# Kernel tuning notes

Hardware: AMD Instinct MI355X
Metric: run time of the kernel (lower is better)

Reference implementation:

```python
import jax, jax.numpy as jnp
import numpy as np

N = 100000   # nodes
E = 1600000  # edges
IN_DIM = 165
HID = 64
OUT = 2


def setup_inputs() -> dict:
    key = jax.random.key(0)
    ks = jax.random.split(key, 6)
    x = jax.random.normal(ks[0], (N, IN_DIM), dtype=jnp.float32)
    edge_index = jax.random.randint(ks[1], (2, E), 0, N, dtype=jnp.int32)
    # Glorot-ish init for the two GCNConv linear weights + post-agg biases
    W1 = jax.random.normal(ks[2], (IN_DIM, HID), dtype=jnp.float32) * (1.0 / np.sqrt(IN_DIM))
    b1 = jnp.zeros((HID,), dtype=jnp.float32)
    W2 = jax.random.normal(ks[3], (HID, OUT), dtype=jnp.float32) * (1.0 / np.sqrt(HID))
    b2 = jnp.zeros((OUT,), dtype=jnp.float32)
    return {"x": x, "edge_index": edge_index, "W1": W1, "b1": b1, "W2": W2, "b2": b2}


def _gcn_norm(src, dst, n):
    # PyG GCNConv default: add self-loops, symmetric normalization
    deg = jax.ops.segment_sum(jnp.ones_like(src, dtype=jnp.float32), dst, num_segments=n)
    deg = deg + 1.0  # self-loop
    dinv = jax.lax.rsqrt(deg)
    edge_norm = dinv[src] * dinv[dst]          # [E]
    self_norm = dinv * dinv                    # [N], norm for self-loop edges
    return edge_norm, self_norm


def _gcn_conv(h, W, b, src, dst, edge_norm, self_norm, n):
    hw = h @ W                                 # [N, F_out] transform first (PyG order)
    msgs = hw[src] * edge_norm[:, None]        # gather + scale  [E, F_out]
    agg = jax.ops.segment_sum(msgs, dst, num_segments=n)
    agg = agg + hw * self_norm[:, None]        # self-loop contribution
    return agg + b


def reference(x, edge_index, W1, b1, W2, b2):
    src, dst = edge_index[0], edge_index[1]
    edge_norm, self_norm = _gcn_norm(src, dst, N)
    h = _gcn_conv(x, W1, b1, src, dst, edge_norm, self_norm, N)
    h = jax.nn.relu(h)
    # F.dropout with training=False (eval) is identity
    out = _gcn_conv(h, W2, b2, src, dst, edge_norm, self_norm, N)
    return out
```

## Files before the change

### kernel.cpp

```cpp
#include <hip/hip_runtime.h>
#include <hip/hip_fp16.h>

#define N_NODES 100000
#define N_EDGES 1600000
#define IN_DIM 165
#define HID 64
#define OUT_DIM 2
#define NB ((N_NODES + 127) / 128)
#define CAP 3072
#define EPB 4096
#define BIN_BLOCKS ((N_EDGES + EPB - 1) / EPB)
#define KP 64
#define XST 72

typedef _Float16 f16x8 __attribute__((ext_vector_type(8)));
typedef float f32x4 __attribute__((ext_vector_type(4)));

__global__ __launch_bounds__(512) void k_bin(const int* __restrict__ src,
                                             const int* __restrict__ dst,
                                             int* __restrict__ bcnt,
                                             unsigned int* __restrict__ rec) {
    __shared__ int hist[NB];
    __shared__ int rstart[NB];
    __shared__ int gbase[NB];
    __shared__ int cur[NB];
    __shared__ int tsum[512];
    __shared__ unsigned int lrec[EPB];
    __shared__ unsigned short lbkt[EPB];
    const int tid = threadIdx.x;
    for (int b = tid; b < NB; b += 512) { hist[b] = 0; cur[b] = 0; }
    __syncthreads();
    const int e0 = blockIdx.x * EPB;
    const int total = min(EPB, N_EDGES - e0);
    for (int j = tid; j < total; j += 512)
        atomicAdd(&hist[dst[e0 + j] >> 7], 1);
    __syncthreads();
    int own[2];
    int s = 0;
    #pragma unroll
    for (int u = 0; u < 2; ++u) {
        int idx = tid * 2 + u;
        own[u] = s;
        s += (idx < NB) ? hist[idx] : 0;
    }
    tsum[tid] = s;
    __syncthreads();
    for (int off = 1; off < 512; off <<= 1) {
        int t = (tid >= off) ? tsum[tid - off] : 0;
        __syncthreads();
        tsum[tid] += t;
        __syncthreads();
    }
    int prev = (tid > 0) ? tsum[tid - 1] : 0;
    #pragma unroll
    for (int u = 0; u < 2; ++u) {
        int idx = tid * 2 + u;
        if (idx < NB) rstart[idx] = prev + own[u];
    }
    for (int b = tid; b < NB; b += 512)
        if (hist[b] > 0) gbase[b] = atomicAdd(&bcnt[b], hist[b]);
    __syncthreads();
    for (int j = tid; j < total; j += 512) {
        int d = dst[e0 + j], sv = src[e0 + j];
        int b = d >> 7;
        int off = atomicAdd(&cur[b], 1);
        int slot = rstart[b] + off;
        lrec[slot] = (unsigned int)sv | ((unsigned int)(d & 127) << 17);
        lbkt[slot] = (unsigned short)b;
    }
    __syncthreads();
    for (int slot = tid; slot < total; slot += 512) {
        int b = lbkt[slot];
        int pos = gbase[b] + (slot - rstart[b]);
        rec[(size_t)b * CAP + pos] = lrec[slot];
    }
}

__global__ void k_bscan(const int* __restrict__ bcnt, int* __restrict__ bbase,
                        int* __restrict__ row_ptr) {
    __shared__ int lds[1024];
    const int tid = threadIdx.x;
    int v = (tid < NB) ? bcnt[tid] : 0;
    lds[tid] = v;
    __syncthreads();
    for (int off = 1; off < 1024; off <<= 1) {
        int t = (tid >= off) ? lds[tid - off] : 0;
        __syncthreads();
        lds[tid] += t;
        __syncthreads();
    }
    if (tid < NB) bbase[tid] = lds[tid] - v;
    if (tid == 0) row_ptr[N_NODES] = N_EDGES;
}

__global__ __launch_bounds__(256) void k_sort2(const int* __restrict__ bcnt,
                                               const int* __restrict__ bbase,
                                               const unsigned int* __restrict__ rec,
                                               int* __restrict__ row_ptr,
                                               float* __restrict__ dinv,
                                               int* __restrict__ esrc) {
    __shared__ int hist[128];
    __shared__ int scn[128];
    __shared__ int cur[128];
    const int tid = threadIdx.x;
    const int b = blockIdx.x;
    const int n0 = b << 7;
    if (tid < 128) { hist[tid] = 0; cur[tid] = 0; }
    __syncthreads();
    const int cb = bcnt[b];
    const size_t s0 = (size_t)b * CAP;
    const int gb = bbase[b];
    unsigned int rv[12];
    #pragma unroll
    for (int u = 0; u < 12; ++u) {
        int i = tid + (u << 8);
        rv[u] = 0;
        if (i < cb) {
            rv[u] = rec[s0 + i];
            atomicAdd(&hist[rv[u] >> 17], 1);
        }
    }
    __syncthreads();
    int v = (tid < 128) ? hist[tid] : 0;
    if (tid < 128) scn[tid] = v;
    __syncthreads();
    for (int off = 1; off < 128; off <<= 1) {
        int t = (tid >= off && tid < 128) ? scn[tid - off] : 0;
        __syncthreads();
        if (tid < 128) scn[tid] += t;
        __syncthreads();
    }
    if (tid < 128) {
        int n = n0 + tid;
        if (n < N_NODES) {
            row_ptr[n] = gb + scn[tid] - v;
            dinv[n] = rsqrtf((float)v + 1.0f);
        }
    }
    __syncthreads();
    #pragma unroll
    for (int u = 0; u < 12; ++u) {
        int i = tid + (u << 8);
        if (i < cb) {
            int ld = (int)(rv[u] >> 17);
            int pos = gb + (scn[ld] - hist[ld]) + atomicAdd(&cur[ld], 1);
            esrc[pos] = (int)(rv[u] & 131071u);
        }
    }
}

__global__ __launch_bounds__(256) void k_gemm1(const float* __restrict__ x,
                                               const float* __restrict__ W1,
                                               const float* __restrict__ dinv,
                                               __half* __restrict__ hw1h) {
    __shared__ __align__(16) _Float16 xs[32 * XST];
    __shared__ __align__(16) _Float16 wsf[8 * 64 * 8];
    const int tid = threadIdx.x;
    const int lane = tid & 63;
    const int wave = tid >> 6;
    const int lg = lane >> 4;
    const int lm = lane & 15;
    const int mt = wave >> 1;
    const int nh = wave & 1;
    const int base = blockIdx.x * 32;
    const int nrows = min(32, N_NODES - base);

    const int srow = tid >> 3;
    const int sseg = (tid & 7) * 8;
    const int src_r = min(srow, nrows - 1);
    const float* xrow = x + (size_t)(base + src_r) * IN_DIM;
    const bool rvalid = (srow < nrows);

    f32x4 acc[2] = {};

    for (int p = 0; p < 3; ++p) {
        const int k0 = p * KP;
        #pragma unroll
        for (int u = 0; u < 8; ++u) {
            int kk = sseg + u;
            int k = k0 + kk;
            float v = xrow[min(k, IN_DIM - 1)];
            xs[srow * XST + kk] = (rvalid && k < IN_DIM) ? (_Float16)v : (_Float16)0.f;
        }
        #pragma unroll
        for (int it = 0; it < 2; ++it) {
            int idx = tid + 256 * it;
            int g = idx >> 6;
            int n = idx & 63;
            f16x8 frag;
            #pragma unroll
            for (int j = 0; j < 8; ++j) {
                int k = k0 + 8 * g + j;
                float v = W1[(size_t)min(k, IN_DIM - 1) * HID + n];
                frag[j] = (k < IN_DIM) ? (_Float16)v : (_Float16)0.f;
            }
            *(f16x8*)&wsf[((g << 6) + n) * 8] = frag;
        }
        __syncthreads();
        #pragma unroll
        for (int s = 0; s < 2; ++s) {
            f16x8 af = *(const f16x8*)&xs[(16 * mt + lm) * XST + 32 * s + 8 * lg];
            #pragma unroll
            for (int nb = 0; nb < 2; ++nb) {
                int nt = 2 * nh + nb;
                f16x8 bf = *(const f16x8*)&wsf[(((s << 2) + lg) * 64 + (nt << 4) + lm) * 8];
                acc[nb] = __builtin_amdgcn_mfma_f32_16x16x32_f16(af, bf, acc[nb], 0, 0, 0);
            }
        }
        __syncthreads();
    }

    #pragma unroll
    for (int r = 0; r < 4; ++r) {
        int grow = base + 16 * mt + 4 * lg + r;
        if (grow < N_NODES) {
            float dv = dinv[grow];
            #pragma unroll
            for (int nb = 0; nb < 2; ++nb) {
                int nt = 2 * nh + nb;
                hw1h[(size_t)grow * HID + (nt << 4) + lm] = __float2half(acc[nb][r] * dv);
            }
        }
    }
}

__global__ __launch_bounds__(256) void k_gather1(const int* __restrict__ row_ptr,
                                                 const int* __restrict__ esrc,
                                                 const __half* __restrict__ hw1h,
                                                 const float* __restrict__ dinv,
                                                 const float* __restrict__ b1,
                                                 const float* __restrict__ W2,
                                                 float* __restrict__ hw2s) {
    __shared__ float w2s[HID * OUT_DIM];
    __shared__ float b1s[HID];
    const int tid = threadIdx.x;
    if (tid < HID * OUT_DIM) w2s[tid] = W2[tid];
    if (tid < HID) b1s[tid] = b1[tid];
    __syncthreads();

    const int node = blockIdx.x * 16 + (tid >> 4);
    const int q = tid & 15;
    if (node >= N_NODES) return;
    const int beg = row_ptr[node], end = row_ptr[node + 1];
    float4 acc = {0.f, 0.f, 0.f, 0.f};
    int i = beg;
    for (; i + 7 < end; i += 8) {
        uint2 u[8];
        #pragma unroll
        for (int e = 0; e < 8; ++e) {
            int s = esrc[i + e];
            u[e] = *(const uint2*)&hw1h[(size_t)s * HID + 4 * q];
        }
        #pragma unroll
        for (int e = 0; e < 8; ++e) {
            float2 a0 = __half22float2(*(const __half2*)&u[e].x);
            float2 a1 = __half22float2(*(const __half2*)&u[e].y);
            acc.x += a0.x; acc.y += a0.y; acc.z += a1.x; acc.w += a1.y;
        }
    }
    for (; i + 3 < end; i += 4) {
        uint2 u[4];
        #pragma unroll
        for (int e = 0; e < 4; ++e) {
            int s = esrc[i + e];
            u[e] = *(const uint2*)&hw1h[(size_t)s * HID + 4 * q];
        }
        #pragma unroll
        for (int e = 0; e < 4; ++e) {
            float2 a0 = __half22float2(*(const __half2*)&u[e].x);
            float2 a1 = __half22float2(*(const __half2*)&u[e].y);
            acc.x += a0.x; acc.y += a0.y; acc.z += a1.x; acc.w += a1.y;
        }
    }
    for (; i < end; ++i) {
        int s = esrc[i];
        uint2 u = *(const uint2*)&hw1h[(size_t)s * HID + 4 * q];
        float2 a0 = __half22float2(*(const __half2*)&u.x);
        float2 a1 = __half22float2(*(const __half2*)&u.y);
        acc.x += a0.x; acc.y += a0.y; acc.z += a1.x; acc.w += a1.y;
    }
    const float dv = dinv[node];
    uint2 us = *(const uint2*)&hw1h[(size_t)node * HID + 4 * q];
    float2 h0 = __half22float2(*(const __half2*)&us.x);
    float2 h1 = __half22float2(*(const __half2*)&us.y);
    float h[4];
    h[0] = fmaxf(dv * (acc.x + h0.x) + b1s[4 * q + 0], 0.f);
    h[1] = fmaxf(dv * (acc.y + h0.y) + b1s[4 * q + 1], 0.f);
    h[2] = fmaxf(dv * (acc.z + h1.x) + b1s[4 * q + 2], 0.f);
    h[3] = fmaxf(dv * (acc.w + h1.y) + b1s[4 * q + 3], 0.f);
    float s0 = 0.f, s1 = 0.f;
    #pragma unroll
    for (int k = 0; k < 4; ++k) {
        int j = 4 * q + k;
        s0 += h[k] * w2s[2 * j + 0];
        s1 += h[k] * w2s[2 * j + 1];
    }
    #pragma unroll
    for (int off = 8; off >= 1; off >>= 1) {
        s0 += __shfl_down(s0, off, 16);
        s1 += __shfl_down(s1, off, 16);
    }
    if (q == 0) {
        hw2s[(size_t)node * 2 + 0] = s0 * dv;
        hw2s[(size_t)node * 2 + 1] = s1 * dv;
    }
}

__global__ __launch_bounds__(256) void k_gather2(const int* __restrict__ row_ptr,
                                                 const int* __restrict__ esrc,
                                                 const float* __restrict__ hw2s,
                                                 const float* __restrict__ dinv,
                                                 const float* __restrict__ b2,
                                                 float* __restrict__ out) {
    const int tid = threadIdx.x;
    const int node = blockIdx.x * 64 + (tid >> 2);
    const int e4 = tid & 3;
    if (node >= N_NODES) return;
    const int beg = row_ptr[node], end = row_ptr[node + 1];
    float a0 = 0.f, a1 = 0.f;
    for (int i = beg + e4; i < end; i += 4) {
        int s = esrc[i];
        float2 v = *(const float2*)&hw2s[(size_t)s * 2];
        a0 += v.x;
        a1 += v.y;
    }
    a0 += __shfl_xor(a0, 1, 4); a0 += __shfl_xor(a0, 2, 4);
    a1 += __shfl_xor(a1, 1, 4); a1 += __shfl_xor(a1, 2, 4);
    if (e4 == 0) {
        float dv = dinv[node];
        float2 sv = *(const float2*)&hw2s[(size_t)node * 2];
        out[(size_t)node * 2 + 0] = dv * (a0 + sv.x) + b2[0];
        out[(size_t)node * 2 + 1] = dv * (a1 + sv.y) + b2[1];
    }
}

extern "C" void kernel_launch(void* const* d_in, const int* in_sizes, int n_in,
                              void* d_out, int out_size, void* d_ws, size_t ws_size,
                              hipStream_t stream) {
    const float* x  = (const float*)d_in[0];
    const int*   ei = (const int*)d_in[1];
    const float* W1 = (const float*)d_in[2];
    const float* b1 = (const float*)d_in[3];
    const float* W2 = (const float*)d_in[4];
    const float* b2 = (const float*)d_in[5];
    float* out = (float*)d_out;
    const int* src = ei;
    const int* dst = ei + N_EDGES;

    char* w = (char*)d_ws;
    __half* hw1h   = (__half*)w;          w += (size_t)N_NODES * HID * 2;
    int*   esrc    = (int*)w;             w += (size_t)N_EDGES * 4;
    unsigned int* rec = (unsigned int*)w; w += (size_t)NB * CAP * 4;
    float* dinv    = (float*)w;           w += (size_t)N_NODES * 4;
    float* hw2s    = (float*)w;           w += (size_t)N_NODES * 2 * 4;
    int*   row_ptr = (int*)w;             w += (size_t)(N_NODES + 1) * 4;
    int*   bcnt    = (int*)w;             w += (size_t)NB * 4;
    int*   bbase   = (int*)w;             w += (size_t)NB * 4;

    hipMemsetAsync(bcnt, 0, NB * sizeof(int), stream);

    k_bin<<<BIN_BLOCKS, 512, 0, stream>>>(src, dst, bcnt, rec);
    k_bscan<<<1, 1024, 0, stream>>>(bcnt, bbase, row_ptr);
    k_sort2<<<NB, 256, 0, stream>>>(bcnt, bbase, rec, row_ptr, dinv, esrc);
    k_gemm1<<<(N_NODES + 31) / 32, 256, 0, stream>>>(x, W1, dinv, hw1h);
    k_gather1<<<(N_NODES + 15) / 16, 256, 0, stream>>>(row_ptr, esrc, hw1h, dinv, b1, W2, hw2s);
    k_gather2<<<(N_NODES + 63) / 64, 256, 0, stream>>>(row_ptr, esrc, hw2s, dinv, b2, out);
}
```

Measured before the change: 117.5 us.

## Fold bucket prefix scan into sort kernel and deepen gather unroll

Removes the separate single-block scan kernel. Each sort block now computes its own global base by reducing the bucket counts that precede it, so one launch and one dependency step are dropped. To support this, the sort kernel moves to 512 threads with 6 records per thread. The redundant reduction repeats up to about 782 loads per block. Separately, the first gather loop gets a 16-edge unrolled stage so more independent loads are in flight, at the cost of more registers.

```diff
diff --git a/kernel.cpp b/kernel.cpp
--- a/kernel.cpp
+++ b/kernel.cpp
@@ -76,25 +76,7 @@
     }
 }
 
-__global__ void k_bscan(const int* __restrict__ bcnt, int* __restrict__ bbase,
-                        int* __restrict__ row_ptr) {
-    __shared__ int lds[1024];
-    const int tid = threadIdx.x;
-    int v = (tid < NB) ? bcnt[tid] : 0;
-    lds[tid] = v;
-    __syncthreads();
-    for (int off = 1; off < 1024; off <<= 1) {
-        int t = (tid >= off) ? lds[tid - off] : 0;
-        __syncthreads();
-        lds[tid] += t;
-        __syncthreads();
-    }
-    if (tid < NB) bbase[tid] = lds[tid] - v;
-    if (tid == 0) row_ptr[N_NODES] = N_EDGES;
-}
-
-__global__ __launch_bounds__(256) void k_sort2(const int* __restrict__ bcnt,
-                                               const int* __restrict__ bbase,
+__global__ __launch_bounds__(512) void k_sort2(const int* __restrict__ bcnt,
                                                const unsigned int* __restrict__ rec,
                                                int* __restrict__ row_ptr,
                                                float* __restrict__ dinv,
@@ -102,18 +84,26 @@
     __shared__ int hist[128];
     __shared__ int scn[128];
     __shared__ int cur[128];
+    __shared__ int tsum[512];
     const int tid = threadIdx.x;
     const int b = blockIdx.x;
     const int n0 = b << 7;
     if (tid < 128) { hist[tid] = 0; cur[tid] = 0; }
-    __syncthreads();
+    int part = 0;
+    for (int j = tid; j < b; j += 512) part += bcnt[j];
+    tsum[tid] = part;
+    __syncthreads();
+    for (int off = 256; off >= 1; off >>= 1) {
+        if (tid < off) tsum[tid] += tsum[tid + off];
+        __syncthreads();
+    }
+    const int gb = tsum[0];
     const int cb = bcnt[b];
     const size_t s0 = (size_t)b * CAP;
-    const int gb = bbase[b];
-    unsigned int rv[12];
-    #pragma unroll
-    for (int u = 0; u < 12; ++u) {
-        int i = tid + (u << 8);
+    unsigned int rv[6];
+    #pragma unroll
+    for (int u = 0; u < 6; ++u) {
+        int i = tid + (u << 9);
         rv[u] = 0;
         if (i < cb) {
             rv[u] = rec[s0 + i];
@@ -137,10 +127,11 @@
             dinv[n] = rsqrtf((float)v + 1.0f);
         }
     }
-    __syncthreads();
-    #pragma unroll
-    for (int u = 0; u < 12; ++u) {
-        int i = tid + (u << 8);
+    if (b == NB - 1 && tid == 0) row_ptr[N_NODES] = N_EDGES;
+    __syncthreads();
+    #pragma unroll
+    for (int u = 0; u < 6; ++u) {
+        int i = tid + (u << 9);
         if (i < cb) {
             int ld = (int)(rv[u] >> 17);
             int pos = gb + (scn[ld] - hist[ld]) + atomicAdd(&cur[ld], 1);
@@ -244,6 +235,20 @@
     const int beg = row_ptr[node], end = row_ptr[node + 1];
     float4 acc = {0.f, 0.f, 0.f, 0.f};
     int i = beg;
+    for (; i + 15 < end; i += 16) {
+        uint2 u[16];
+        #pragma unroll
+        for (int e = 0; e < 16; ++e) {
+            int s = esrc[i + e];
+            u[e] = *(const uint2*)&hw1h[(size_t)s * HID + 4 * q];
+        }
+        #pragma unroll
+        for (int e = 0; e < 16; ++e) {
+            float2 a0 = __half22float2(*(const __half2*)&u[e].x);
+            float2 a1 = __half22float2(*(const __half2*)&u[e].y);
+            acc.x += a0.x; acc.y += a0.y; acc.z += a1.x; acc.w += a1.y;
+        }
+    }
     for (; i + 7 < end; i += 8) {
         uint2 u[8];
         #pragma unroll
@@ -355,13 +360,11 @@
     float* hw2s    = (float*)w;           w += (size_t)N_NODES * 2 * 4;
     int*   row_ptr = (int*)w;             w += (size_t)(N_NODES + 1) * 4;
     int*   bcnt    = (int*)w;             w += (size_t)NB * 4;
-    int*   bbase   = (int*)w;             w += (size_t)NB * 4;
 
     hipMemsetAsync(bcnt, 0, NB * sizeof(int), stream);
 
     k_bin<<<BIN_BLOCKS, 512, 0, stream>>>(src, dst, bcnt, rec);
-    k_bscan<<<1, 1024, 0, stream>>>(bcnt, bbase, row_ptr);
-    k_sort2<<<NB, 256, 0, stream>>>(bcnt, bbase, rec, row_ptr, dinv, esrc);
+    k_sort2<<<NB, 512, 0, stream>>>(bcnt, rec, row_ptr, dinv, esrc);
     k_gemm1<<<(N_NODES + 31) / 32, 256, 0, stream>>>(x, W1, dinv, hw1h);
     k_gather1<<<(N_NODES + 15) / 16, 256, 0, stream>>>(row_ptr, esrc, hw1h, dinv, b1, W2, hw2s);
     k_gather2<<<(N_NODES + 63) / 64, 256, 0, stream>>>(row_ptr, esrc, hw2s, dinv, b2, out);
```

New measurement: 121.4 us. 1.03x slower.
